# Kernel optimization log

Hardware: AMD Instinct MI355X
Metric: run time of the kernel (lower is better)

The kernel has to match this reference:

```python
import jax, jax.numpy as jnp
import numpy as np

N = 30000          # num nodes
E = 480000         # num edges (avg degree 16)
K = 3              # Chebyshev filter order
IN = 128           # input feature dim
LAMBDA_MAX = 2.0   # PyG default spectral bound
DIMS = [IN, 16, 32, 64, 128, 256, 512]


def setup_inputs() -> dict:
    key = jax.random.key(0)
    ks = jax.random.split(key, 20)
    inp = {
        "x": jax.random.normal(ks[0], (N, IN), dtype=jnp.float32),
        "edge_index": jax.random.randint(ks[1], (2, E), 0, N, dtype=jnp.int32),
        "edge_weight": jax.random.uniform(ks[2], (E,), dtype=jnp.float32),
        "batch": jnp.arange(N, dtype=jnp.int32),  # each node its own graph -> pooling is identity
    }
    for i in range(6):
        fi, fo = DIMS[i], DIMS[i + 1]
        scale = 1.0 / np.sqrt(fi * K)
        inp[f"W{i+1}"] = jax.random.normal(ks[3 + 2 * i], (K, fi, fo), dtype=jnp.float32) * scale
        inp[f"b{i+1}"] = jnp.zeros((fo,), dtype=jnp.float32)
    inp["fc_w"] = jax.random.normal(ks[16], (512, 3), dtype=jnp.float32) * 0.05
    inp["fc_b"] = jnp.zeros((3,), dtype=jnp.float32)
    return inp


def _cheb_conv(x, row, col, w_off, diag, W, b):
    """ChebConv with rw-normalized, rescaled Laplacian Lhat = 2L/lmax - I.
    Lhat @ v = scatter(w_off * v[row] -> col) + diag * v."""
    def lmv(v):
        return jax.ops.segment_sum(w_off[:, None] * v[row], col, num_segments=N) + diag * v
    Tx0 = x
    out = Tx0 @ W[0]
    Tx1 = lmv(x)
    out = out + Tx1 @ W[1]
    for k in range(2, W.shape[0]):
        Tx2 = 2.0 * lmv(Tx1) - Tx0
        out = out + Tx2 @ W[k]
        Tx0, Tx1 = Tx1, Tx2
    return out + b


def _forward(x, edge_index, edge_weight, batch, Ws, bs, fc_w, fc_b):
    row, col = edge_index[0], edge_index[1]
    # random-walk Laplacian L = I - D^{-1} A, then Lhat = 2L/lmax - I
    deg = jax.ops.segment_sum(edge_weight, row, num_segments=N)
    deg_inv = jnp.where(deg > 0, 1.0 / deg, 0.0)
    w_off = -(2.0 / LAMBDA_MAX) * deg_inv[row] * edge_weight   # off-diagonal entries of Lhat
    diag = 2.0 / LAMBDA_MAX - 1.0                               # diagonal entry of Lhat (0 for lmax=2)
    h = x
    for W, b in zip(Ws, bs):
        h = _cheb_conv(h, row, col, w_off, diag, W, b)
        h = jax.ops.segment_max(h, batch, num_segments=N)  # global_max_pool; identity since batch=arange
        h = jax.nn.softplus(h)
    return h @ fc_w + fc_b


def reference(x, edge_index, edge_weight, batch, W1, b1, W2, b2, W3, b3, W4, b4, W5, b5, W6, b6, fc_w, fc_b):
    Ws = [W1, W2, W3, W4, W5, W6]
    bs = [b1, b2, b3, b4, b5, b6]
    return _forward(x, edge_index, edge_weight, batch, Ws, bs, fc_w, fc_b)
```

## Files before the change

kernel.cpp:

```cpp
#include <hip/hip_runtime.h>
#include <math.h>
#include <stdint.h>

#define NN 30000
#define EE 480000
#define MPAD 30080
#define SCAN_B 30

typedef __attribute__((ext_vector_type(8))) short short8;
typedef __attribute__((ext_vector_type(4))) float floatx4;

__device__ __forceinline__ float b2f(ushort u) {
    union { uint u; float f; } c; c.u = ((uint)u) << 16; return c.f;
}
__device__ __forceinline__ ushort f2b(float f) {
    union { float f; uint u; } c; c.f = f;
    uint u = c.u;
    uint r = (u + 0x7FFFu + ((u >> 16) & 1u)) >> 16;
    return (ushort)r;
}
__device__ __forceinline__ float softplus_f(float x) {
    float a = fabsf(x) * 1.44269504f;
    float t = __builtin_amdgcn_exp2f(-a);
    float l = __builtin_amdgcn_logf(1.f + t);
    return fmaxf(x, 0.f) + 0.69314718f * l;
}

__device__ __forceinline__ void gld_lds16(const void* g, void* lds) {
    __builtin_amdgcn_global_load_lds(
        (__attribute__((address_space(1))) void*)(uintptr_t)(g),
        (__attribute__((address_space(3))) void*)(uint32_t)(uintptr_t)(lds),
        16, 0, 0);
}

__device__ __forceinline__ void barrier_raw() {
    __asm__ volatile("s_barrier" ::: "memory");
}
template <int N>
__device__ __forceinline__ void waitcnt_vm() {
    if constexpr (N == 0) __asm__ volatile("s_waitcnt vmcnt(0)" ::: "memory");
    else if constexpr (N == 2) __asm__ volatile("s_waitcnt vmcnt(2)" ::: "memory");
    else if constexpr (N == 3) __asm__ volatile("s_waitcnt vmcnt(3)" ::: "memory");
    else if constexpr (N == 4) __asm__ volatile("s_waitcnt vmcnt(4)" ::: "memory");
    else if constexpr (N == 8) __asm__ volatile("s_waitcnt vmcnt(8)" ::: "memory");
}

__global__ void edge_pass1(const int* __restrict__ row, const int* __restrict__ col,
                           const float* __restrict__ ew,
                           float* __restrict__ deg, int* __restrict__ counts, int E) {
    int e = blockIdx.x * blockDim.x + threadIdx.x;
    if (e >= E) return;
    atomicAdd(&deg[row[e]], ew[e]);
    atomicAdd(&counts[col[e]], 1);
}

__global__ __launch_bounds__(256) void scan_part(const int* __restrict__ counts,
                                                 int* __restrict__ bsums, int N) {
    __shared__ int s[256];
    int t = threadIdx.x;
    int base = blockIdx.x * 1024 + t * 4;
    int4 v = make_int4(0, 0, 0, 0);
    if (base + 3 < N) v = *(const int4*)(counts + base);
    else {
        if (base + 0 < N) v.x = counts[base + 0];
        if (base + 1 < N) v.y = counts[base + 1];
        if (base + 2 < N) v.z = counts[base + 2];
        if (base + 3 < N) v.w = counts[base + 3];
    }
    s[t] = v.x + v.y + v.z + v.w;
    __syncthreads();
    for (int off = 1; off < 256; off <<= 1) {
        int x = (t >= off) ? s[t - off] : 0;
        __syncthreads();
        s[t] += x;
        __syncthreads();
    }
    if (t == 255) bsums[blockIdx.x] = s[255];
}

__global__ void scan_tops(int* __restrict__ bsums) {
    int lane = threadIdx.x & 63;
    int orig = (lane < SCAN_B) ? bsums[lane] : 0;
    int v = orig;
    #pragma unroll
    for (int off = 1; off < 64; off <<= 1) {
        int x = __shfl_up(v, off);
        if (lane >= off) v += x;
    }
    if (lane < SCAN_B) bsums[lane] = v - orig;
}

__global__ __launch_bounds__(256) void scan_final(
        const int* __restrict__ counts, const int* __restrict__ bsums,
        int* __restrict__ offs, int* __restrict__ cursor, int N) {
    __shared__ int s[256];
    int t = threadIdx.x;
    int base = blockIdx.x * 1024 + t * 4;
    int4 v = make_int4(0, 0, 0, 0);
    if (base + 3 < N) v = *(const int4*)(counts + base);
    else {
        if (base + 0 < N) v.x = counts[base + 0];
        if (base + 1 < N) v.y = counts[base + 1];
        if (base + 2 < N) v.z = counts[base + 2];
        if (base + 3 < N) v.w = counts[base + 3];
    }
    int sum = v.x + v.y + v.z + v.w;
    s[t] = sum;
    __syncthreads();
    for (int off = 1; off < 256; off <<= 1) {
        int x = (t >= off) ? s[t - off] : 0;
        __syncthreads();
        s[t] += x;
        __syncthreads();
    }
    int tb = s[t] - sum + bsums[blockIdx.x];
    int4 o;
    o.x = tb;
    o.y = o.x + v.x;
    o.z = o.y + v.y;
    o.w = o.z + v.z;
    if (base + 3 < N) {
        *(int4*)(offs + base) = o;
        *(int4*)(cursor + base) = o;
    } else {
        if (base + 0 < N) { offs[base + 0] = o.x; cursor[base + 0] = o.x; }
        if (base + 1 < N) { offs[base + 1] = o.y; cursor[base + 1] = o.y; }
        if (base + 2 < N) { offs[base + 2] = o.z; cursor[base + 2] = o.z; }
        if (base + 3 < N) { offs[base + 3] = o.w; cursor[base + 3] = o.w; }
    }
    if (blockIdx.x == 0 && t == 0) offs[N] = EE;
}

__global__ void edge_pass2(const int* __restrict__ row, const int* __restrict__ col,
                           const float* __restrict__ ew, const float* __restrict__ deg,
                           int* __restrict__ cursor,
                           int* __restrict__ csr_row, float* __restrict__ csr_w, int E) {
    int e = blockIdx.x * blockDim.x + threadIdx.x;
    if (e >= E) return;
    int r = row[e];
    float d = deg[r];
    float wv = (d > 0.f) ? (-ew[e] / d) : 0.f;
    int pos = atomicAdd(&cursor[col[e]], 1);
    csr_row[pos] = r;
    csr_w[pos] = wv;
}

__global__ void copy_x_kernel(const float* __restrict__ x, ushort* __restrict__ out,
                              int total4) {
    int idx = blockIdx.x * blockDim.x + threadIdx.x;
    if (idx >= total4) return;
    float4 v = *(const float4*)(x + idx * 4);
    ushort4 o;
    o.x = f2b(v.x); o.y = f2b(v.y); o.z = f2b(v.z); o.w = f2b(v.w);
    *(ushort4*)(out + idx * 4) = o;
}

__global__ void wconv_all(const float* __restrict__ W1, const float* __restrict__ W2,
                          const float* __restrict__ W3, const float* __restrict__ W4,
                          const float* __restrict__ W5, const float* __restrict__ W6,
                          ushort* __restrict__ B1, ushort* __restrict__ B2,
                          ushort* __restrict__ B3, ushort* __restrict__ B4,
                          ushort* __restrict__ B5, ushort* __restrict__ B6) {
    int idx = blockIdx.x * blockDim.x + threadIdx.x;
    if (idx < 6144) {
        int row = idx >> 7, k = idx & 127;
        int j = row >> 4, n = row & 15;
        B1[idx] = f2b(W1[(j * 128 + k) * 16 + n]);
    } else if (idx < 8192) {
        int t = idx - 6144; int n = t >> 6, k = t & 63;
        B2[t] = f2b(k < 48 ? W2[k * 32 + n] : 0.f);
    } else if (idx < 14336) {
        int t = idx - 8192; int n = t / 96, k = t - n * 96;
        B3[t] = f2b(W3[k * 64 + n]);
    } else if (idx < 38912) {
        int t = idx - 14336; int n = t / 192, k = t - n * 192;
        B4[t] = f2b(W4[k * 128 + n]);
    } else if (idx < 137216) {
        int t = idx - 38912; int n = t / 384, k = t - n * 384;
        B5[t] = f2b(W5[k * 256 + n]);
    } else if (idx < 530432) {
        int t = idx - 137216; int n = t / 768, k = t - n * 768;
        B6[t] = f2b(W6[k * 512 + n]);
    }
}

template <int FI>
__global__ __launch_bounds__(256) void lmv_bf16(
        const ushort* __restrict__ A, ushort* __restrict__ Out,
        const ushort* __restrict__ Sub, int ldi, int ldo,
        const int* __restrict__ offs, const int* __restrict__ rows,
        const float* __restrict__ w, float scale, int N) {
    constexpr int NPW = 64 / FI;
    int wave = threadIdx.x >> 6;
    int lane = threadIdx.x & 63;
    int sub = lane / FI;
    int fbase = lane & (FI - 1);
    int node = blockIdx.x * (4 * NPW) + wave * NPW + sub;
    if (node >= N) return;
    int e0 = offs[node], e1 = offs[node + 1];
    float acc[4];
    #pragma unroll
    for (int c = 0; c < 4; ++c) acc[c] = 0.f;
    int e = e0;
    for (; e + 4 <= e1; e += 4) {
        int r0 = rows[e], r1 = rows[e + 1], r2 = rows[e + 2], r3 = rows[e + 3];
        float w0 = w[e], w1 = w[e + 1], w2 = w[e + 2], w3 = w[e + 3];
        acc[0] += w0 * b2f(A[(size_t)r0 * ldi + fbase]);
        acc[1] += w1 * b2f(A[(size_t)r1 * ldi + fbase]);
        acc[2] += w2 * b2f(A[(size_t)r2 * ldi + fbase]);
        acc[3] += w3 * b2f(A[(size_t)r3 * ldi + fbase]);
    }
    for (; e < e1; ++e)
        acc[0] += w[e] * b2f(A[(size_t)rows[e] * ldi + fbase]);
    float a = (acc[0] + acc[1]) + (acc[2] + acc[3]);
    ushort* o = Out + (size_t)node * ldo + fbase;
    if (Sub) {
        const ushort* s = Sub + (size_t)node * ldo + fbase;
        *o = f2b(scale * a - b2f(*s));
    } else {
        *o = f2b(scale * a);
    }
}

__global__ __launch_bounds__(256) void lmv_l1_final(
        const ushort* __restrict__ Z,
        const ushort* __restrict__ Y,
        const float* __restrict__ b,
        ushort* __restrict__ Out,
        const int* __restrict__ offs, const int* __restrict__ rows,
        const float* __restrict__ w, int N) {
    int wave = threadIdx.x >> 6;
    int lane = threadIdx.x & 63;
    int sub = lane >> 4, f = lane & 15;
    int node = blockIdx.x * 16 + wave * 4 + sub;
    if (node >= N) return;
    int e0 = offs[node], e1 = offs[node + 1];
    const ushort* Z2 = Z + 16;
    float acc[4];
    #pragma unroll
    for (int c = 0; c < 4; ++c) acc[c] = 0.f;
    int e = e0;
    for (; e + 4 <= e1; e += 4) {
        int r0 = rows[e], r1 = rows[e + 1], r2 = rows[e + 2], r3 = rows[e + 3];
        float w0 = w[e], w1 = w[e + 1], w2 = w[e + 2], w3 = w[e + 3];
        acc[0] += w0 * b2f(Z2[(size_t)r0 * 32 + f]);
        acc[1] += w1 * b2f(Z2[(size_t)r1 * 32 + f]);
        acc[2] += w2 * b2f(Z2[(size_t)r2 * 32 + f]);
        acc[3] += w3 * b2f(Z2[(size_t)r3 * 32 + f]);
    }
    for (; e < e1; ++e)
        acc[0] += w[e] * b2f(Z2[(size_t)rows[e] * 32 + f]);
    float z3 = (acc[0] + acc[1]) + (acc[2] + acc[3]);
    float y0 = b2f(Y[(size_t)node * 48 + f]);
    float y2 = b2f(Y[(size_t)node * 48 + 32 + f]);
    float z1 = b2f(Z[(size_t)node * 32 + f]);
    float v = y0 + z1 + 2.f * z3 - y2 + b[f];
    Out[(size_t)node * 64 + f] = f2b(softplus_f(v));
}

template <int VEC>
__global__ __launch_bounds__(256) void lmv_vec(
        const ushort* __restrict__ A, ushort* __restrict__ Out,
        const ushort* __restrict__ Sub, int ld,
        const int* __restrict__ offs, const int* __restrict__ rows,
        const float* __restrict__ w, float scale) {
    constexpr int CH = 8;
    int node = blockIdx.x * 4 + (threadIdx.x >> 6);
    int lane = threadIdx.x & 63;
    int fbase = lane * VEC;
    int e0 = __builtin_amdgcn_readfirstlane(offs[node]);
    int e1 = __builtin_amdgcn_readfirstlane(offs[node + 1]);
    float acc[CH][VEC];
    #pragma unroll
    for (int c = 0; c < CH; ++c)
        #pragma unroll
        for (int v = 0; v < VEC; ++v) acc[c][v] = 0.f;
    int e = e0;
    for (; e + CH <= e1; e += CH) {
        #pragma unroll
        for (int c = 0; c < CH; ++c) {
            int r = rows[e + c];
            float we = w[e + c];
            const ushort* pr = A + (size_t)r * ld + fbase;
            if constexpr (VEC == 4) {
                ushort4 u = *(const ushort4*)pr;
                acc[c][0] += we * b2f(u.x); acc[c][1] += we * b2f(u.y);
                acc[c][2] += we * b2f(u.z); acc[c][3] += we * b2f(u.w);
            } else if constexpr (VEC == 2) {
                ushort2 u = *(const ushort2*)pr;
                acc[c][0] += we * b2f(u.x); acc[c][1] += we * b2f(u.y);
            } else {
                acc[c][0] += we * b2f(*pr);
            }
        }
    }
    for (; e < e1; ++e) {
        int c = e & (CH - 1);
        int r = rows[e];
        float we = w[e];
        const ushort* pr = A + (size_t)r * ld + fbase;
        if constexpr (VEC == 4) {
            ushort4 u = *(const ushort4*)pr;
            acc[c][0] += we * b2f(u.x); acc[c][1] += we * b2f(u.y);
            acc[c][2] += we * b2f(u.z); acc[c][3] += we * b2f(u.w);
        } else if constexpr (VEC == 2) {
            ushort2 u = *(const ushort2*)pr;
            acc[c][0] += we * b2f(u.x); acc[c][1] += we * b2f(u.y);
        } else {
            acc[c][0] += we * b2f(*pr);
        }
    }
    #pragma unroll
    for (int c = 1; c < CH; ++c)
        #pragma unroll
        for (int v = 0; v < VEC; ++v) acc[0][v] += acc[c][v];
    ushort* o = Out + (size_t)node * ld + fbase;
    if (Sub) {
        const ushort* s = Sub + (size_t)node * ld + fbase;
        ushort tmp[VEC];
        #pragma unroll
        for (int v = 0; v < VEC; ++v) tmp[v] = f2b(scale * acc[0][v] - b2f(s[v]));
        #pragma unroll
        for (int v = 0; v < VEC; ++v) o[v] = tmp[v];
    } else {
        #pragma unroll
        for (int v = 0; v < VEC; ++v) o[v] = f2b(scale * acc[0][v]);
    }
}

template <int BN, bool ACT = true>
__global__ __launch_bounds__(256) void gemm_mfma(
        const ushort* __restrict__ A, int lda, int K,
        const ushort* __restrict__ Bt,
        const float* __restrict__ bias,
        ushort* __restrict__ Out, int ldo) {
    constexpr int BM = 128, BK = 32;
    constexpr int SM = 32;
    constexpr int FM = 2;
    constexpr int FN = BN / 16;
    constexpr int CB = BN / 16;
    constexpr int WAITN = (BN == 64) ? 3 : 2;
    __shared__ __align__(16) ushort As[2][BM][BK];
    __shared__ __align__(16) ushort Bs[2][BN][BK];
    int tid = threadIdx.x;
    int wv = tid >> 6, ln = tid & 63;
    int q = ln >> 4, r16 = ln & 15;
    int m0 = blockIdx.x * BM;

    int lrow = ln >> 2;
    int gseg = (ln & 3) ^ ((ln >> 3) & 3);
    const ushort* Abase = A + (size_t)(m0 + lrow) * lda + gseg * 8;
    const ushort* Bbase = Bt + (size_t)lrow * K + gseg * 8;

    floatx4 acc[FM][FN];
    #pragma unroll
    for (int i = 0; i < FM; ++i)
        #pragma unroll
        for (int j = 0; j < FN; ++j) acc[i][j] = (floatx4){0.f, 0.f, 0.f, 0.f};

    int sw = (q ^ ((r16 >> 1) & 3)) * 8;
    int aoff[FM], boff[FN];
    #pragma unroll
    for (int i = 0; i < FM; ++i) aoff[i] = (wv * SM + i * 16 + r16) * BK + sw;
    #pragma unroll
    for (int j = 0; j < FN; ++j) boff[j] = (j * 16 + r16) * BK + sw;

    auto stage = [&](int b, int k0) {
        gld_lds16(Abase + (size_t)(wv * 16) * lda + k0, &As[b][wv * 16][0]);
        gld_lds16(Abase + (size_t)(64 + wv * 16) * lda + k0, &As[b][64 + wv * 16][0]);
        if constexpr (CB == 4) {
            gld_lds16(Bbase + (size_t)(wv * 16) * K + k0, &Bs[b][wv * 16][0]);
        } else {
            if (wv < CB) gld_lds16(Bbase + (size_t)(wv * 16) * K + k0, &Bs[b][wv * 16][0]);
        }
    };
    auto compute = [&](int b) {
        const ushort* ldsA = &As[b][0][0];
        const ushort* ldsB = &Bs[b][0][0];
        short8 af[FM], bf[FN];
        #pragma unroll
        for (int i = 0; i < FM; ++i) af[i] = *(const short8*)(ldsA + aoff[i]);
        #pragma unroll
        for (int j = 0; j < FN; ++j) bf[j] = *(const short8*)(ldsB + boff[j]);
        #pragma unroll
        for (int i = 0; i < FM; ++i)
            #pragma unroll
            for (int j = 0; j < FN; ++j)
                acc[i][j] = __builtin_amdgcn_mfma_f32_16x16x32_bf16(
                    af[i], bf[j], acc[i][j], 0, 0, 0);
    };

    int nIter = K / BK;
    stage(0, 0);
    for (int i = 0; i < nIter; ++i) {
        int cur = i & 1;
        barrier_raw();
        if (i + 1 < nIter) {
            stage(cur ^ 1, (i + 1) * BK);
            waitcnt_vm<WAITN>();
        } else {
            waitcnt_vm<0>();
        }
        barrier_raw();
        compute(cur);
    }
    #pragma unroll
    for (int i = 0; i < FM; ++i) {
        #pragma unroll
        for (int j = 0; j < FN; ++j) {
            int n = j * 16 + r16;
            float bv = ACT ? bias[n] : 0.f;
            #pragma unroll
            for (int r = 0; r < 4; ++r) {
                int m = m0 + wv * SM + i * 16 + q * 4 + r;
                float v = acc[i][j][r] + bv;
                Out[(size_t)m * ldo + n] = f2b(ACT ? softplus_f(v) : v);
            }
        }
    }
}

template <bool FC = false, int YB = 0>
__global__ __launch_bounds__(256) void gemm_bk64(
        const ushort* __restrict__ A, int lda, int K,
        const ushort* __restrict__ Bt,
        const float* __restrict__ bias,
        ushort* __restrict__ Out, int ldo,
        const float* __restrict__ fcw, float* __restrict__ fcout) {
    constexpr int BM = 128, BN = 128, BK = 64;
    __shared__ __align__(16) ushort As[2][BM][BK];
    __shared__ __align__(16) ushort Bs[2][BN][BK];
    int tid = threadIdx.x;
    int wv = tid >> 6, ln = tid & 63;
    int wm = wv & 1, wn = wv >> 1;
    int q = ln >> 4, r16 = ln & 15;
    int yb = blockIdx.x & ((1 << YB) - 1);
    int xb = blockIdx.x >> YB;
    int m0 = xb * BM;
    int n0 = yb * BN;

    int lrow8 = ln >> 3, slds = ln & 7;
    int gseg = slds ^ lrow8;
    const ushort* Abase = A + (size_t)(m0 + lrow8) * lda + gseg * 8;
    const ushort* Bbase = Bt + (size_t)(n0 + lrow8) * K + gseg * 8;

    floatx4 acc[4][4];
    #pragma unroll
    for (int i = 0; i < 4; ++i)
        #pragma unroll
        for (int j = 0; j < 4; ++j) acc[i][j] = (floatx4){0.f, 0.f, 0.f, 0.f};

    int r7 = r16 & 7;
    int aoff[2][4], boff[2][4];
    #pragma unroll
    for (int s = 0; s < 2; ++s) {
        int segp = ((s * 4 + q) ^ r7) * 8;
        #pragma unroll
        for (int i = 0; i < 4; ++i) {
            aoff[s][i] = (wm * 64 + i * 16 + r16) * BK + segp;
            boff[s][i] = (wn * 64 + i * 16 + r16) * BK + segp;
        }
    }

    auto stage = [&](int b, int k0) {
        #pragma unroll
        for (int g = 0; g < 4; ++g)
            gld_lds16(Abase + (size_t)(wv * 8 + g * 32) * lda + k0,
                      &As[b][wv * 8 + g * 32][0]);
        #pragma unroll
        for (int g = 0; g < 4; ++g)
            gld_lds16(Bbase + (size_t)(wv * 8 + g * 32) * K + k0,
                      &Bs[b][wv * 8 + g * 32][0]);
    };
    auto compute = [&](int b) {
        const ushort* ldsA = &As[b][0][0];
        const ushort* ldsB = &Bs[b][0][0];
        #pragma unroll
        for (int s = 0; s < 2; ++s) {
            short8 af[4], bf[4];
            #pragma unroll
            for (int i = 0; i < 4; ++i) af[i] = *(const short8*)(ldsA + aoff[s][i]);
            #pragma unroll
            for (int j = 0; j < 4; ++j) bf[j] = *(const short8*)(ldsB + boff[s][j]);
            #pragma unroll
            for (int i = 0; i < 4; ++i)
                #pragma unroll
                for (int j = 0; j < 4; ++j)
                    acc[i][j] = __builtin_amdgcn_mfma_f32_16x16x32_bf16(
                        af[i], bf[j], acc[i][j], 0, 0, 0);
        }
    };

    int nIter = K / BK;
    stage(0, 0);
    for (int i = 0; i < nIter; ++i) {
        int cur = i & 1;
        barrier_raw();
        if (i + 1 < nIter) {
            stage(cur ^ 1, (i + 1) * BK);
            waitcnt_vm<8>();
        } else {
            waitcnt_vm<0>();
        }
        barrier_raw();
        compute(cur);
    }

    if constexpr (FC) {
        int pb = yb * 2 + wn;
        #pragma unroll
        for (int i = 0; i < 4; ++i) {
            #pragma unroll
            for (int r = 0; r < 4; ++r) {
                float p0 = 0.f, p1 = 0.f, p2 = 0.f;
                #pragma unroll
                for (int j = 0; j < 4; ++j) {
                    int n = n0 + wn * 64 + j * 16 + r16;
                    float v = softplus_f(acc[i][j][r] + bias[n]);
                    p0 += v * fcw[n * 3 + 0];
                    p1 += v * fcw[n * 3 + 1];
                    p2 += v * fcw[n * 3 + 2];
                }
                #pragma unroll
                for (int off = 1; off < 16; off <<= 1) {
                    p0 += __shfl_xor(p0, off);
                    p1 += __shfl_xor(p1, off);
                    p2 += __shfl_xor(p2, off);
                }
                if (r16 == 0) {
                    int m = m0 + wm * 64 + i * 16 + q * 4 + r;
                    float* dst = fcout + ((size_t)pb * MPAD + m) * 3;
                    dst[0] = p0; dst[1] = p1; dst[2] = p2;
                }
            }
        }
    } else {
        #pragma unroll
        for (int i = 0; i < 4; ++i) {
            #pragma unroll
            for (int j = 0; j < 4; ++j) {
                int n = n0 + wn * 64 + j * 16 + r16;
                float bv = bias[n];
                #pragma unroll
                for (int r = 0; r < 4; ++r) {
                    int m = m0 + wm * 64 + i * 16 + q * 4 + r;
                    Out[(size_t)m * ldo + n] = f2b(softplus_f(acc[i][j][r] + bv));
                }
            }
        }
    }
}

__global__ __launch_bounds__(256) void fc_reduce(
        const float* __restrict__ part, const float* __restrict__ fcb,
        float* __restrict__ out) {
    int idx = blockIdx.x * blockDim.x + threadIdx.x;
    if (idx >= NN * 3) return;
    int c = idx - (idx / 3) * 3;
    float s = 0.f;
    #pragma unroll
    for (int pb = 0; pb < 8; ++pb)
        s += part[(size_t)pb * MPAD * 3 + idx];
    out[idx] = s + fcb[c];
}

static inline size_t align256(size_t x) { return (x + 255) & ~(size_t)255; }

extern "C" void kernel_launch(void* const* d_in, const int* in_sizes, int n_in,
                              void* d_out, int out_size, void* d_ws, size_t ws_size,
                              hipStream_t stream) {
    const float* x   = (const float*)d_in[0];
    const int*   ei  = (const int*)d_in[1];
    const float* ew  = (const float*)d_in[2];
    const float* W[6]  = { (const float*)d_in[4],  (const float*)d_in[6],
                           (const float*)d_in[8],  (const float*)d_in[10],
                           (const float*)d_in[12], (const float*)d_in[14] };
    const float* Bv[6] = { (const float*)d_in[5],  (const float*)d_in[7],
                           (const float*)d_in[9],  (const float*)d_in[11],
                           (const float*)d_in[13], (const float*)d_in[15] };
    const float* fc_w = (const float*)d_in[16];
    const float* fc_b = (const float*)d_in[17];
    float* out = (float*)d_out;

    const int* e_row = ei;
    const int* e_col = ei + EE;

    const int fi_arr[5]   = { 16, 32, 64, 128, 256 };
    const int fo_arr[5]   = { 32, 64, 128, 256, 512 };
    const int Kpad_arr[5] = { 64, 96, 192, 384, 768 };
    const int ldo_arr[5]  = { 96, 192, 384, 768, 512 };

    char* p = (char*)d_ws;
    float* deg    = (float*)p; p += align256((size_t)NN * 4);
    int*   counts = (int*)p;   p += align256((size_t)NN * 4);
    int*   offs   = (int*)p;   p += align256((size_t)(NN + 1) * 4);
    int*   cursor = (int*)p;   p += align256((size_t)NN * 4);
    int*   bsums  = (int*)p;   p += align256((size_t)SCAN_B * 4);
    int*   csr_r  = (int*)p;   p += align256((size_t)EE * 4);
    float* csr_w  = (float*)p; p += align256((size_t)EE * 4);
    ushort* Bt1   = (ushort*)p; p += align256((size_t)48 * 128 * 2);
    ushort* Bt[5];
    for (int L = 0; L < 5; ++L) {
        Bt[L] = (ushort*)p;
        p += align256((size_t)fo_arr[L] * Kpad_arr[L] * 2);
    }
    float* fcpart = (float*)p; p += align256((size_t)8 * MPAD * 3 * 4);
    ushort* xb   = (ushort*)p; p += align256((size_t)MPAD * 128 * 2);
    ushort* Ybuf = (ushort*)p; p += align256((size_t)MPAD * 48 * 2);
    ushort* Zbuf = (ushort*)p; p += align256((size_t)MPAD * 32 * 2);
    ushort* buf0 = (ushort*)p; p += align256((size_t)MPAD * 768 * 2);
    ushort* buf1 = (ushort*)p; p += align256((size_t)MPAD * 768 * 2);
    (void)ws_size; (void)n_in; (void)in_sizes; (void)out_size;

    hipMemsetAsync(deg, 0, align256((size_t)NN * 4) + (size_t)NN * 4, stream);

    {
        int blocks = (EE + 255) / 256;
        edge_pass1<<<blocks, 256, 0, stream>>>(e_row, e_col, ew, deg, counts, EE);
        scan_part<<<SCAN_B, 256, 0, stream>>>(counts, bsums, NN);
        scan_tops<<<1, 64, 0, stream>>>(bsums);
        scan_final<<<SCAN_B, 256, 0, stream>>>(counts, bsums, offs, cursor, NN);
        edge_pass2<<<blocks, 256, 0, stream>>>(e_row, e_col, ew, deg, cursor, csr_r, csr_w, EE);
    }

    wconv_all<<<(530432 + 255) / 256, 256, 0, stream>>>(
        W[0], W[1], W[2], W[3], W[4], W[5],
        Bt1, Bt[0], Bt[1], Bt[2], Bt[3], Bt[4]);

    copy_x_kernel<<<(NN * 128 / 4 + 255) / 256, 256, 0, stream>>>(x, xb, NN * 128 / 4);

    gemm_mfma<48, false><<<dim3(MPAD / 128), 256, 0, stream>>>(
        xb, 128, 128, Bt1, nullptr, Ybuf, 48);
    lmv_bf16<32><<<(NN + 7) / 8, 256, 0, stream>>>(
        Ybuf + 16, Zbuf, nullptr, 48, 32, offs, csr_r, csr_w, 1.0f, NN);
    lmv_l1_final<<<(NN + 15) / 16, 256, 0, stream>>>(
        Zbuf, Ybuf, Bv[0], buf1, offs, csr_r, csr_w, NN);

    ushort* Abuf[5] = { buf1, buf0, buf1, buf0, buf1 };
    ushort* Obuf[5] = { buf0, buf1, buf0, buf1, buf0 };

    for (int L = 0; L < 5; ++L) {
        int fi = fi_arr[L];
        int ldA = Kpad_arr[L];
        int ldO = ldo_arr[L];
        ushort* A = Abuf[L];
        ushort* O = Obuf[L];

        switch (fi) {
            case 16:
                lmv_bf16<16><<<(NN + 15) / 16, 256, 0, stream>>>(
                    A, A + fi, nullptr, ldA, ldA, offs, csr_r, csr_w, 1.0f, NN);
                lmv_bf16<16><<<(NN + 15) / 16, 256, 0, stream>>>(
                    A + fi, A + 2 * fi, A, ldA, ldA, offs, csr_r, csr_w, 2.0f, NN);
                break;
            case 32:
                lmv_bf16<32><<<(NN + 7) / 8, 256, 0, stream>>>(
                    A, A + fi, nullptr, ldA, ldA, offs, csr_r, csr_w, 1.0f, NN);
                lmv_bf16<32><<<(NN + 7) / 8, 256, 0, stream>>>(
                    A + fi, A + 2 * fi, A, ldA, ldA, offs, csr_r, csr_w, 2.0f, NN);
                break;
            case 64:
                lmv_vec<1><<<NN / 4, 256, 0, stream>>>(
                    A, A + fi, nullptr, ldA, offs, csr_r, csr_w, 1.0f);
                lmv_vec<1><<<NN / 4, 256, 0, stream>>>(
                    A + fi, A + 2 * fi, A, ldA, offs, csr_r, csr_w, 2.0f);
                break;
            case 128:
                lmv_vec<2><<<NN / 4, 256, 0, stream>>>(
                    A, A + fi, nullptr, ldA, offs, csr_r, csr_w, 1.0f);
                lmv_vec<2><<<NN / 4, 256, 0, stream>>>(
                    A + fi, A + 2 * fi, A, ldA, offs, csr_r, csr_w, 2.0f);
                break;
            default:
                lmv_vec<4><<<NN / 4, 256, 0, stream>>>(
                    A, A + fi, nullptr, ldA, offs, csr_r, csr_w, 1.0f);
                lmv_vec<4><<<NN / 4, 256, 0, stream>>>(
                    A + fi, A + 2 * fi, A, ldA, offs, csr_r, csr_w, 2.0f);
                break;
        }

        int K = Kpad_arr[L];
        switch (fo_arr[L]) {
            case 32:
                gemm_mfma<32><<<dim3(MPAD / 128), 256, 0, stream>>>(
                    A, ldA, K, Bt[L], Bv[L + 1], O, ldO);
                break;
            case 64:
                gemm_mfma<64><<<dim3(MPAD / 128), 256, 0, stream>>>(
                    A, ldA, K, Bt[L], Bv[L + 1], O, ldO);
                break;
            case 128:
                gemm_bk64<false, 0><<<dim3(MPAD / 128), 256, 0, stream>>>(
                    A, ldA, K, Bt[L], Bv[L + 1], O, ldO, nullptr, nullptr);
                break;
            case 256:
                gemm_bk64<false, 1><<<dim3(MPAD / 128 * 2), 256, 0, stream>>>(
                    A, ldA, K, Bt[L], Bv[L + 1], O, ldO, nullptr, nullptr);
                break;
            default:
                gemm_bk64<true, 2><<<dim3(MPAD / 128 * 4), 256, 0, stream>>>(
                    A, ldA, K, Bt[L], Bv[L + 1], nullptr, 0, fc_w, fcpart);
                break;
        }
    }

    fc_reduce<<<(NN * 3 + 255) / 256, 256, 0, stream>>>(fcpart, fc_b, out);
}
```

Baseline: 485.9 us.

## Interleave CSR row/weight pairs, fuse prep kernels, fold scan tops, unroll gathers

Stores CSR row indices and weights as interleaved int2 pairs, so each gathered edge needs one 8-byte load instead of two separate 4-byte loads from different arrays. Merges the x-to-bf16 conversion and weight conversion into a single prep kernel. Folds the block-sum scan into scan_final to drop one launch. Widens the bf16 gather loops from 4 to 8 accumulators to allow more loads in flight. The cost is extra register pressure in the small-feature lmv kernels, and each of the 30 scan_final blocks now redundantly rescans the block sums.

```diff
diff --git a/kernel.cpp b/kernel.cpp
--- a/kernel.cpp
+++ b/kernel.cpp
@@ -24,6 +24,9 @@
     float t = __builtin_amdgcn_exp2f(-a);
     float l = __builtin_amdgcn_logf(1.f + t);
     return fmaxf(x, 0.f) + 0.69314718f * l;
+}
+__device__ __forceinline__ float i2f(int i) {
+    union { int i; float f; } c; c.i = i; return c.f;
 }
 
 __device__ __forceinline__ void gld_lds16(const void* g, void* lds) {
@@ -78,23 +81,23 @@
     if (t == 255) bsums[blockIdx.x] = s[255];
 }
 
-__global__ void scan_tops(int* __restrict__ bsums) {
-    int lane = threadIdx.x & 63;
-    int orig = (lane < SCAN_B) ? bsums[lane] : 0;
-    int v = orig;
-    #pragma unroll
-    for (int off = 1; off < 64; off <<= 1) {
-        int x = __shfl_up(v, off);
-        if (lane >= off) v += x;
-    }
-    if (lane < SCAN_B) bsums[lane] = v - orig;
-}
-
 __global__ __launch_bounds__(256) void scan_final(
         const int* __restrict__ counts, const int* __restrict__ bsums,
         int* __restrict__ offs, int* __restrict__ cursor, int N) {
     __shared__ int s[256];
+    __shared__ int sbase;
     int t = threadIdx.x;
+    if (t < 64) {
+        int lane = t;
+        int orig = (lane < SCAN_B) ? bsums[lane] : 0;
+        int v = orig;
+        #pragma unroll
+        for (int off = 1; off < 64; off <<= 1) {
+            int x = __shfl_up(v, off);
+            if (lane >= off) v += x;
+        }
+        if (lane == (int)blockIdx.x) sbase = v - orig;
+    }
     int base = blockIdx.x * 1024 + t * 4;
     int4 v = make_int4(0, 0, 0, 0);
     if (base + 3 < N) v = *(const int4*)(counts + base);
@@ -113,7 +116,7 @@
         s[t] += x;
         __syncthreads();
     }
-    int tb = s[t] - sum + bsums[blockIdx.x];
+    int tb = s[t] - sum + sbase;
     int4 o;
     o.x = tb;
     o.y = o.x + v.x;
@@ -133,35 +136,36 @@
 
 __global__ void edge_pass2(const int* __restrict__ row, const int* __restrict__ col,
                            const float* __restrict__ ew, const float* __restrict__ deg,
-                           int* __restrict__ cursor,
-                           int* __restrict__ csr_row, float* __restrict__ csr_w, int E) {
+                           int* __restrict__ cursor, int2* __restrict__ csr_rw, int E) {
     int e = blockIdx.x * blockDim.x + threadIdx.x;
     if (e >= E) return;
     int r = row[e];
     float d = deg[r];
     float wv = (d > 0.f) ? (-ew[e] / d) : 0.f;
     int pos = atomicAdd(&cursor[col[e]], 1);
-    csr_row[pos] = r;
-    csr_w[pos] = wv;
-}
-
-__global__ void copy_x_kernel(const float* __restrict__ x, ushort* __restrict__ out,
-                              int total4) {
-    int idx = blockIdx.x * blockDim.x + threadIdx.x;
-    if (idx >= total4) return;
-    float4 v = *(const float4*)(x + idx * 4);
-    ushort4 o;
-    o.x = f2b(v.x); o.y = f2b(v.y); o.z = f2b(v.z); o.w = f2b(v.w);
-    *(ushort4*)(out + idx * 4) = o;
-}
-
-__global__ void wconv_all(const float* __restrict__ W1, const float* __restrict__ W2,
-                          const float* __restrict__ W3, const float* __restrict__ W4,
-                          const float* __restrict__ W5, const float* __restrict__ W6,
-                          ushort* __restrict__ B1, ushort* __restrict__ B2,
-                          ushort* __restrict__ B3, ushort* __restrict__ B4,
-                          ushort* __restrict__ B5, ushort* __restrict__ B6) {
-    int idx = blockIdx.x * blockDim.x + threadIdx.x;
+    int2 rw;
+    rw.x = r;
+    rw.y = __float_as_int(wv);
+    csr_rw[pos] = rw;
+}
+
+#define XTOT 960000
+__global__ void prep_all(const float* __restrict__ x, ushort* __restrict__ xb,
+                         const float* __restrict__ W1, const float* __restrict__ W2,
+                         const float* __restrict__ W3, const float* __restrict__ W4,
+                         const float* __restrict__ W5, const float* __restrict__ W6,
+                         ushort* __restrict__ B1, ushort* __restrict__ B2,
+                         ushort* __restrict__ B3, ushort* __restrict__ B4,
+                         ushort* __restrict__ B5, ushort* __restrict__ B6) {
+    int gid = blockIdx.x * blockDim.x + threadIdx.x;
+    if (gid < XTOT) {
+        float4 v = *(const float4*)(x + gid * 4);
+        ushort4 o;
+        o.x = f2b(v.x); o.y = f2b(v.y); o.z = f2b(v.z); o.w = f2b(v.w);
+        *(ushort4*)(xb + gid * 4) = o;
+        return;
+    }
+    int idx = gid - XTOT;
     if (idx < 6144) {
         int row = idx >> 7, k = idx & 127;
         int j = row >> 4, n = row & 15;
@@ -188,8 +192,8 @@
 __global__ __launch_bounds__(256) void lmv_bf16(
         const ushort* __restrict__ A, ushort* __restrict__ Out,
         const ushort* __restrict__ Sub, int ldi, int ldo,
-        const int* __restrict__ offs, const int* __restrict__ rows,
-        const float* __restrict__ w, float scale, int N) {
+        const int* __restrict__ offs, const int2* __restrict__ csr,
+        float scale, int N) {
     constexpr int NPW = 64 / FI;
     int wave = threadIdx.x >> 6;
     int lane = threadIdx.x & 63;
@@ -198,21 +202,23 @@
     int node = blockIdx.x * (4 * NPW) + wave * NPW + sub;
     if (node >= N) return;
     int e0 = offs[node], e1 = offs[node + 1];
-    float acc[4];
-    #pragma unroll
-    for (int c = 0; c < 4; ++c) acc[c] = 0.f;
+    float acc[8];
+    #pragma unroll
+    for (int c = 0; c < 8; ++c) acc[c] = 0.f;
     int e = e0;
-    for (; e + 4 <= e1; e += 4) {
-        int r0 = rows[e], r1 = rows[e + 1], r2 = rows[e + 2], r3 = rows[e + 3];
-        float w0 = w[e], w1 = w[e + 1], w2 = w[e + 2], w3 = w[e + 3];
-        acc[0] += w0 * b2f(A[(size_t)r0 * ldi + fbase]);
-        acc[1] += w1 * b2f(A[(size_t)r1 * ldi + fbase]);
-        acc[2] += w2 * b2f(A[(size_t)r2 * ldi + fbase]);
-        acc[3] += w3 * b2f(A[(size_t)r3 * ldi + fbase]);
-    }
-    for (; e < e1; ++e)
-        acc[0] += w[e] * b2f(A[(size_t)rows[e] * ldi + fbase]);
-    float a = (acc[0] + acc[1]) + (acc[2] + acc[3]);
+    for (; e + 8 <= e1; e += 8) {
+        #pragma unroll
+        for (int c = 0; c < 8; ++c) {
+            int2 rw = csr[e + c];
+            acc[c] += i2f(rw.y) * b2f(A[(size_t)rw.x * ldi + fbase]);
+        }
+    }
+    for (; e < e1; ++e) {
+        int2 rw = csr[e];
+        acc[0] += i2f(rw.y) * b2f(A[(size_t)rw.x * ldi + fbase]);
+    }
+    float a = ((acc[0] + acc[1]) + (acc[2] + acc[3])) +
+              ((acc[4] + acc[5]) + (acc[6] + acc[7]));
     ushort* o = Out + (size_t)node * ldo + fbase;
     if (Sub) {
         const ushort* s = Sub + (size_t)node * ldo + fbase;
@@ -227,8 +233,7 @@
         const ushort* __restrict__ Y,
         const float* __restrict__ b,
         ushort* __restrict__ Out,
-        const int* __restrict__ offs, const int* __restrict__ rows,
-        const float* __restrict__ w, int N) {
+        const int* __restrict__ offs, const int2* __restrict__ csr, int N) {
     int wave = threadIdx.x >> 6;
     int lane = threadIdx.x & 63;
     int sub = lane >> 4, f = lane & 15;
@@ -236,21 +241,23 @@
     if (node >= N) return;
     int e0 = offs[node], e1 = offs[node + 1];
     const ushort* Z2 = Z + 16;
-    float acc[4];
-    #pragma unroll
-    for (int c = 0; c < 4; ++c) acc[c] = 0.f;
+    float acc[8];
+    #pragma unroll
+    for (int c = 0; c < 8; ++c) acc[c] = 0.f;
     int e = e0;
-    for (; e + 4 <= e1; e += 4) {
-        int r0 = rows[e], r1 = rows[e + 1], r2 = rows[e + 2], r3 = rows[e + 3];
-        float w0 = w[e], w1 = w[e + 1], w2 = w[e + 2], w3 = w[e + 3];
-        acc[0] += w0 * b2f(Z2[(size_t)r0 * 32 + f]);
-        acc[1] += w1 * b2f(Z2[(size_t)r1 * 32 + f]);
-        acc[2] += w2 * b2f(Z2[(size_t)r2 * 32 + f]);
-        acc[3] += w3 * b2f(Z2[(size_t)r3 * 32 + f]);
-    }
-    for (; e < e1; ++e)
-        acc[0] += w[e] * b2f(Z2[(size_t)rows[e] * 32 + f]);
-    float z3 = (acc[0] + acc[1]) + (acc[2] + acc[3]);
+    for (; e + 8 <= e1; e += 8) {
+        #pragma unroll
+        for (int c = 0; c < 8; ++c) {
+            int2 rw = csr[e + c];
+            acc[c] += i2f(rw.y) * b2f(Z2[(size_t)rw.x * 32 + f]);
+        }
+    }
+    for (; e < e1; ++e) {
+        int2 rw = csr[e];
+        acc[0] += i2f(rw.y) * b2f(Z2[(size_t)rw.x * 32 + f]);
+    }
+    float z3 = ((acc[0] + acc[1]) + (acc[2] + acc[3])) +
+               ((acc[4] + acc[5]) + (acc[6] + acc[7]));
     float y0 = b2f(Y[(size_t)node * 48 + f]);
     float y2 = b2f(Y[(size_t)node * 48 + 32 + f]);
     float z1 = b2f(Z[(size_t)node * 32 + f]);
@@ -262,8 +269,7 @@
 __global__ __launch_bounds__(256) void lmv_vec(
         const ushort* __restrict__ A, ushort* __restrict__ Out,
         const ushort* __restrict__ Sub, int ld,
-        const int* __restrict__ offs, const int* __restrict__ rows,
-        const float* __restrict__ w, float scale) {
+        const int* __restrict__ offs, const int2* __restrict__ csr, float scale) {
     constexpr int CH = 8;
     int node = blockIdx.x * 4 + (threadIdx.x >> 6);
     int lane = threadIdx.x & 63;
@@ -279,8 +285,9 @@
     for (; e + CH <= e1; e += CH) {
         #pragma unroll
         for (int c = 0; c < CH; ++c) {
-            int r = rows[e + c];
-            float we = w[e + c];
+            int2 rw = csr[e + c];
+            int r = rw.x;
+            float we = i2f(rw.y);
             const ushort* pr = A + (size_t)r * ld + fbase;
             if constexpr (VEC == 4) {
                 ushort4 u = *(const ushort4*)pr;
@@ -296,8 +303,9 @@
     }
     for (; e < e1; ++e) {
         int c = e & (CH - 1);
-        int r = rows[e];
-        float we = w[e];
+        int2 rw = csr[e];
+        int r = rw.x;
+        float we = i2f(rw.y);
         const ushort* pr = A + (size_t)r * ld + fbase;
         if constexpr (VEC == 4) {
             ushort4 u = *(const ushort4*)pr;
@@ -596,8 +604,7 @@
     int*   offs   = (int*)p;   p += align256((size_t)(NN + 1) * 4);
     int*   cursor = (int*)p;   p += align256((size_t)NN * 4);
     int*   bsums  = (int*)p;   p += align256((size_t)SCAN_B * 4);
-    int*   csr_r  = (int*)p;   p += align256((size_t)EE * 4);
-    float* csr_w  = (float*)p; p += align256((size_t)EE * 4);
+    int2*  csr_rw = (int2*)p;  p += align256((size_t)EE * 8);
     ushort* Bt1   = (ushort*)p; p += align256((size_t)48 * 128 * 2);
     ushort* Bt[5];
     for (int L = 0; L < 5; ++L) {
@@ -618,23 +625,20 @@
         int blocks = (EE + 255) / 256;
         edge_pass1<<<blocks, 256, 0, stream>>>(e_row, e_col, ew, deg, counts, EE);
         scan_part<<<SCAN_B, 256, 0, stream>>>(counts, bsums, NN);
-        scan_tops<<<1, 64, 0, stream>>>(bsums);
         scan_final<<<SCAN_B, 256, 0, stream>>>(counts, bsums, offs, cursor, NN);
-        edge_pass2<<<blocks, 256, 0, stream>>>(e_row, e_col, ew, deg, cursor, csr_r, csr_w, EE);
-    }
-
-    wconv_all<<<(530432 + 255) / 256, 256, 0, stream>>>(
-        W[0], W[1], W[2], W[3], W[4], W[5],
+        edge_pass2<<<blocks, 256, 0, stream>>>(e_row, e_col, ew, deg, cursor, csr_rw, EE);
+    }
+
+    prep_all<<<(XTOT + 530432 + 255) / 256, 256, 0, stream>>>(
+        x, xb, W[0], W[1], W[2], W[3], W[4], W[5],
         Bt1, Bt[0], Bt[1], Bt[2], Bt[3], Bt[4]);
-
-    copy_x_kernel<<<(NN * 128 / 4 + 255) / 256, 256, 0, stream>>>(x, xb, NN * 128 / 4);
 
     gemm_mfma<48, false><<<dim3(MPAD / 128), 256, 0, stream>>>(
         xb, 128, 128, Bt1, nullptr, Ybuf, 48);
     lmv_bf16<32><<<(NN + 7) / 8, 256, 0, stream>>>(
-        Ybuf + 16, Zbuf, nullptr, 48, 32, offs, csr_r, csr_w, 1.0f, NN);
+        Ybuf + 16, Zbuf, nullptr, 48, 32, offs, csr_rw, 1.0f, NN);
     lmv_l1_final<<<(NN + 15) / 16, 256, 0, stream>>>(
-        Zbuf, Ybuf, Bv[0], buf1, offs, csr_r, csr_w, NN);
+        Zbuf, Ybuf, Bv[0], buf1, offs, csr_rw, NN);
 
     ushort* Abuf[5] = { buf1, buf0, buf1, buf0, buf1 };
     ushort* Obuf[5] = { buf0, buf1, buf0, buf1, buf0 };
@@ -649,33 +653,33 @@
         switch (fi) {
             case 16:
                 lmv_bf16<16><<<(NN + 15) / 16, 256, 0, stream>>>(
-                    A, A + fi, nullptr, ldA, ldA, offs, csr_r, csr_w, 1.0f, NN);
+                    A, A + fi, nullptr, ldA, ldA, offs, csr_rw, 1.0f, NN);
                 lmv_bf16<16><<<(NN + 15) / 16, 256, 0, stream>>>(
-                    A + fi, A + 2 * fi, A, ldA, ldA, offs, csr_r, csr_w, 2.0f, NN);
+                    A + fi, A + 2 * fi, A, ldA, ldA, offs, csr_rw, 2.0f, NN);
                 break;
             case 32:
                 lmv_bf16<32><<<(NN + 7) / 8, 256, 0, stream>>>(
-                    A, A + fi, nullptr, ldA, ldA, offs, csr_r, csr_w, 1.0f, NN);
+                    A, A + fi, nullptr, ldA, ldA, offs, csr_rw, 1.0f, NN);
                 lmv_bf16<32><<<(NN + 7) / 8, 256, 0, stream>>>(
-                    A + fi, A + 2 * fi, A, ldA, ldA, offs, csr_r, csr_w, 2.0f, NN);
+                    A + fi, A + 2 * fi, A, ldA, ldA, offs, csr_rw, 2.0f, NN);
                 break;
             case 64:
                 lmv_vec<1><<<NN / 4, 256, 0, stream>>>(
-                    A, A + fi, nullptr, ldA, offs, csr_r, csr_w, 1.0f);
+                    A, A + fi, nullptr, ldA, offs, csr_rw, 1.0f);
                 lmv_vec<1><<<NN / 4, 256, 0, stream>>>(
-                    A + fi, A + 2 * fi, A, ldA, offs, csr_r, csr_w, 2.0f);
+                    A + fi, A + 2 * fi, A, ldA, offs, csr_rw, 2.0f);
                 break;
             case 128:
                 lmv_vec<2><<<NN / 4, 256, 0, stream>>>(
-                    A, A + fi, nullptr, ldA, offs, csr_r, csr_w, 1.0f);
+                    A, A + fi, nullptr, ldA, offs, csr_rw, 1.0f);
                 lmv_vec<2><<<NN / 4, 256, 0, stream>>>(
-                    A + fi, A + 2 * fi, A, ldA, offs, csr_r, csr_w, 2.0f);
+                    A + fi, A + 2 * fi, A, ldA, offs, csr_rw, 2.0f);
                 break;
             default:
                 lmv_vec<4><<<NN / 4, 256, 0, stream>>>(
-                    A, A + fi, nullptr, ldA, offs, csr_r, csr_w, 1.0f);
+                    A, A + fi, nullptr, ldA, offs, csr_rw, 1.0f);
                 lmv_vec<4><<<NN / 4, 256, 0, stream>>>(
-                    A + fi, A + 2 * fi, A, ldA, offs, csr_r, csr_w, 2.0f);
+                    A + fi, A + 2 * fi, A, ldA, offs, csr_rw, 2.0f);
                 break;
         }
 
```

New measurement: 489.5 us, median of 2. About the same (+0.8%).
